# Performance work log

Hardware: AMD Instinct MI355X
Metric: run time of the kernel (lower is better)

The kernel has to match this reference:

```python
import jax, jax.numpy as jnp
import numpy as np

N = 100_000   # nodes
D = 128       # feature dim (dim_in == dim_out, residual requires it)
E = 1_600_000 # edges
T = 4         # num_layers; edge_attr (hop distance) in 1..T


def setup_inputs() -> dict:
    key = jax.random.key(0)
    k0, k1, k2, k3, k4 = jax.random.split(key, 5)
    x = jax.random.normal(k0, (N, D), dtype=jnp.float32)
    edge_index = jax.random.randint(k1, (2, E), 0, N, dtype=jnp.int32)
    edge_attr = jax.random.randint(k2, (E,), 1, T + 1, dtype=jnp.int32)  # hop k in [1, T]
    W = jax.random.normal(k3, (T, D, D), dtype=jnp.float32) * (1.0 / np.sqrt(D))
    nu = jax.random.normal(k4, (T, T), dtype=jnp.float32) * 0.1  # nu[k-1, t]
    return {"x": x, "edge_index": edge_index, "edge_attr": edge_attr, "W": W, "nu": nu}


def _gcn_edge_coef(edge_index, mask, n):
    """Symmetric GCN normalization 1/sqrt(deg_src*deg_dst) restricted to masked edges."""
    src, dst = edge_index[0], edge_index[1]
    deg_s = jax.ops.segment_sum(mask, src, num_segments=n)
    deg_d = jax.ops.segment_sum(mask, dst, num_segments=n)
    inv = lambda d: jnp.where(d > 0, jax.lax.rsqrt(jnp.maximum(d, 1.0)), 0.0)
    return mask * inv(deg_s)[src] * inv(deg_d)[dst]  # [E]


def reference(x, edge_index, edge_attr, W, nu):
    n = x.shape[0]
    T_layers = nu.shape[1]
    src, dst = edge_index[0], edge_index[1]
    # Precompute per-hop normalized edge coefficients (A(k) masks as weights -> static shapes)
    coefs = [_gcn_edge_coef(edge_index, (edge_attr == k).astype(x.dtype), n)
             for k in range(1, T_layers + 1)]
    hist = [x]  # x_t history
    for t in range(T_layers):
        acc = jnp.zeros_like(x)
        for k in range(1, t + 2):  # k = 1 .. t+1
            h = hist[t + 1 - k] @ W[k - 1]                      # [N, D] linear
            msg = h[src] * coefs[k - 1][:, None]                # gather + weight [E, D]
            agg = jax.ops.segment_sum(msg, dst, num_segments=n) # scatter-sum [N, D]
            acc = acc + nu[k - 1, t] * agg
        xt = hist[t] + jax.nn.relu(acc)                         # residual + ReLU
        # F.normalize(p=2, dim=-1), eps=1e-12 (cfg.gnn.l2norm assumed True)
        xt = xt / jnp.maximum(jnp.linalg.norm(xt, axis=-1, keepdims=True), 1e-12)
        hist.append(xt)
    return hist[-1]
```

## Files before the change

kernel.cpp:

```cpp
#include <hip/hip_runtime.h>

#define DD 128
#define NP 256
#define EB 4096

typedef float4 f4;
typedef __attribute__((ext_vector_type(8))) short bf16x8;
typedef __attribute__((ext_vector_type(4))) float f32x4;

__device__ __forceinline__ short toBf(float f) {
    unsigned u = __float_as_uint(f);
    u += 0x7fff + ((u >> 16) & 1);
    return (short)(u >> 16);
}


__global__ __launch_bounds__(1024) void kAF(const int* __restrict__ ei, int E, int PSZ, int nbA,
                                            int* __restrict__ cntB_D, int* __restrict__ cntB_S,
                                            const float* __restrict__ W, ushort* __restrict__ WT,
                                            int totW, int nPW,
                                            const float* __restrict__ x, ushort* __restrict__ xb,
                                            int n8) {
    __shared__ int hd[NP], hs[NP];
    int tid = threadIdx.x, b = blockIdx.x;
    if (b < nbA) {
        if (tid < NP) { hd[tid] = 0; hs[tid] = 0; }
        __syncthreads();
        int base = b * EB;
        int lim = min(base + EB, E);
        for (int e = base + tid; e < lim; e += 1024) {
            int s = ei[e], d = ei[E + e];
            atomicAdd(&hs[s / PSZ], 1);
            atomicAdd(&hd[d / PSZ], 1);
        }
        __syncthreads();
        if (tid < NP) {
            cntB_D[tid * nbA + b] = hd[tid];
            cntB_S[tid * nbA + b] = hs[tid];
        }
    } else if (b < nbA + nPW) {
        int i = (b - nbA) * 1024 + tid;
        if (i < totW) {
            int k = i >> 14, rem = i & 16383, j = rem >> 7, d = rem & 127;
            WT[i] = (ushort)toBf(W[(size_t)k * 16384 + (size_t)d * DD + j]);
        }
    } else {
        int i = (b - nbA - nPW) * 1024 + tid;
        if (i < n8) {
            const f4* q = (const f4*)(x + (size_t)i * 8);
            f4 lo = q[0], hi = q[1];
            bf16x8 r;
            r[0] = toBf(lo.x); r[1] = toBf(lo.y); r[2] = toBf(lo.z); r[3] = toBf(lo.w);
            r[4] = toBf(hi.x); r[5] = toBf(hi.y); r[6] = toBf(hi.z); r[7] = toBf(hi.w);
            *(bf16x8*)(xb + (size_t)i * 8) = r;
        }
    }
}

__global__ __launch_bounds__(512) void kB1(int* __restrict__ cntB_D, int* __restrict__ cntB_S,
                                           int nbA,
                                           int* __restrict__ partTotD, int* __restrict__ partTotS) {
    __shared__ int sh[512];
    int b = blockIdx.x, tid = threadIdx.x;
    int* cntB = (b < NP) ? cntB_D : cntB_S;
    int* partTot = (b < NP) ? partTotD : partTotS;
    int p = (b < NP) ? b : b - NP;
    int v = (tid < nbA) ? cntB[p * nbA + tid] : 0;
    sh[tid] = v; __syncthreads();
    for (int off = 1; off < 512; off <<= 1) {
        int add = (tid >= off) ? sh[tid - off] : 0;
        __syncthreads(); sh[tid] += add; __syncthreads();
    }
    if (tid < nbA) cntB[p * nbA + tid] = sh[tid] - v;
    if (tid == 511) partTot[p] = sh[511];
}

__global__ __launch_bounds__(1024) void kC(const int* __restrict__ ei, const int* __restrict__ ea,
                                           int E, int N, int T, int PSZ, int nbA,
                                           const int* __restrict__ cntB_D, const int* __restrict__ cntB_S,
                                           const int* __restrict__ partTotD,
                                           const int* __restrict__ partTotS,
                                           int* __restrict__ binD, ushort* __restrict__ binS) {
    __shared__ int pd[NP], ps[NP];
    __shared__ int sc[512];
    int tid = threadIdx.x, b = blockIdx.x;
    if (tid < 512) sc[tid] = (tid < 256) ? partTotD[tid] : partTotS[tid - 256];
    __syncthreads();
    for (int off = 1; off < 256; off <<= 1) {
        int add = 0;
        if (tid < 512 && (tid & 255) >= off) add = sc[tid - off];
        __syncthreads();
        if (tid < 512) sc[tid] += add;
        __syncthreads();
    }
    if (tid < NP) {
        pd[tid] = cntB_D[tid * nbA + b] + (sc[tid] - partTotD[tid]);
        ps[tid] = cntB_S[tid * nbA + b] + (sc[tid + 256] - partTotS[tid]);
    }
    __syncthreads();
    int base = b * EB;
    int lim = min(base + EB, E);
    for (int e = base + tid; e < lim; e += 1024) {
        int s = ei[e], d = ei[E + e], k = ea[e] - 1;
        int dp = d / PSZ, sp = s / PSZ;
        int loc = (d - dp * PSZ) * T + k;
        int posD = atomicAdd(&pd[dp], 1);
        binD[posD] = (loc << 21) | (k << 19) | (k * N + s);
        int posS = atomicAdd(&ps[sp], 1);
        binS[posS] = (ushort)((s - sp * PSZ) * T + k);
    }
}

__global__ __launch_bounds__(512) void kDE(const int* __restrict__ binD,
                                           const ushort* __restrict__ binS,
                                           const int* __restrict__ partTotD,
                                           const int* __restrict__ partTotS,
                                           int N, int T, int PSZ, int M, int E,
                                           int* __restrict__ rowptr, float* __restrict__ isdD2,
                                           int* __restrict__ ep, float* __restrict__ isdS) {
    __shared__ int cnt[4096];
    __shared__ int part[512];
    __shared__ int sc[256];
    int b = blockIdx.x, tid = threadIdx.x;
    bool isD = b < NP;
    int p = isD ? b : b - NP;
    const int* pt = isD ? partTotD : partTotS;
    if (tid < 256) sc[tid] = pt[tid];
    __syncthreads();
    for (int off = 1; off < 256; off <<= 1) {
        int add = (tid < 256 && tid >= off) ? sc[tid - off] : 0;
        __syncthreads();
        if (tid < 256) sc[tid] += add;
        __syncthreads();
    }
    int b1 = sc[p];
    int b0 = b1 - pt[p];
    __syncthreads();
    int nloc = PSZ * T;
    for (int i = tid; i < nloc; i += 512) cnt[i] = 0;
    __syncthreads();
    if (isD) {
        for (int e = b0 + tid; e < b1; e += 512)
            atomicAdd(&cnt[((unsigned)binD[e]) >> 21], 1);
        __syncthreads();
        int CH = (nloc + 511) / 512;
        int c0 = tid * CH, c1 = min(c0 + CH, nloc);
        int s = 0;
        for (int i = c0; i < c1; i++) s += cnt[i];
        part[tid] = s; __syncthreads();
        for (int off = 1; off < 512; off <<= 1) {
            int add = (tid >= off) ? part[tid - off] : 0;
            __syncthreads(); part[tid] += add; __syncthreads();
        }
        int run = ((tid == 0) ? 0 : part[tid - 1]) + b0;
        int gb_base = p * PSZ * T;
        for (int i = c0; i < c1; i++) {
            int v = cnt[i];
            cnt[i] = run;
            int gb = gb_base + i;
            if (gb < M) {
                rowptr[gb] = run;
                isdD2[gb] = rsqrtf((float)max(v, 1));
            }
            run += v;
        }
        __syncthreads();
        for (int e = b0 + tid; e < b1; e += 512) {
            int v = binD[e];
            int pos = atomicAdd(&cnt[((unsigned)v) >> 21], 1);
            ep[pos] = v & 0x1FFFFF;
        }
        if (p == 0 && tid == 0) rowptr[M] = E;
    } else {
        for (int e = b0 + tid; e < b1; e += 512)
            atomicAdd(&cnt[(int)binS[e]], 1);
        __syncthreads();
        int s0 = p * PSZ;
        for (int i = tid; i < nloc; i += 512) {
            int sl = i / T, k = i - sl * T;
            int snode = s0 + sl;
            if (snode < N) isdS[k * N + snode] = rsqrtf((float)max(cnt[i], 1));
        }
    }
}


__global__ __launch_bounds__(256) void k_gemm_multi(
        const ushort* __restrict__ A, const ushort* __restrict__ WTb,
        const float* __restrict__ iskb,
        ushort* __restrict__ d0, ushort* __restrict__ d1,
        ushort* __restrict__ d2, ushort* __restrict__ d3,
        int nk, int N) {
    __shared__ ushort lW[128 * 128];
    int tid = threadIdx.x;
    int wave = tid >> 6;
    int lane = tid & 63;
    int rlo = lane & 15;
    int khi = lane >> 4;
    int r0 = blockIdx.x * 128 + wave * 32;

    int ca[2];
#pragma unroll
    for (int s = 0; s < 2; s++) {
        int r = r0 + s * 16 + rlo;
        ca[s] = r < N ? r : N - 1;
    }
    bf16x8 a[2][4];
#pragma unroll
    for (int s = 0; s < 2; s++)
#pragma unroll
        for (int kk = 0; kk < 4; kk++)
            a[s][kk] = *(const bf16x8*)(A + (size_t)ca[s] * DD + kk * 32 + khi * 8);

#pragma unroll
    for (int i = 0; i < 4; i++) {
        if (i >= nk) break;
        ushort* H = (i == 0) ? d0 : (i == 1) ? d1 : (i == 2) ? d2 : d3;
        const ushort* WT = WTb + (size_t)i * DD * DD;
        const float* isk = iskb + (size_t)i * N;

        __syncthreads();
#pragma unroll
        for (int g8 = 0; g8 < 8; g8++) {
            int g = tid + g8 * 256;
            int row = g >> 4, slot = g & 15;
            bf16x8 v = *(const bf16x8*)(WT + row * DD + slot * 8);
            *(bf16x8*)(lW + row * DD + (slot ^ (row & 7)) * 8) = v;
        }
        __syncthreads();

        f32x4 acc[2][8];
#pragma unroll
        for (int s = 0; s < 2; s++)
#pragma unroll
            for (int j = 0; j < 8; j++) acc[s][j] = (f32x4){0.f, 0.f, 0.f, 0.f};

#pragma unroll
        for (int kk = 0; kk < 4; kk++) {
            int q = kk * 4 + khi;
#pragma unroll
            for (int cg = 0; cg < 8; cg++) {
                int row = cg * 16 + rlo;
                bf16x8 b = *(const bf16x8*)(lW + row * DD + (q ^ (rlo & 7)) * 8);
#pragma unroll
                for (int s = 0; s < 2; s++)
                    acc[s][cg] = __builtin_amdgcn_mfma_f32_16x16x32_bf16(a[s][kk], b, acc[s][cg], 0, 0, 0);
            }
        }

#pragma unroll
        for (int s = 0; s < 2; s++) {
#pragma unroll
            for (int r = 0; r < 4; r++) {
                int row = r0 + s * 16 + khi * 4 + r;
                if (row < N) {
                    float sc = isk[row];
#pragma unroll
                    for (int cg = 0; cg < 8; cg++)
                        H[(size_t)row * DD + cg * 16 + rlo] = (ushort)toBf(sc * acc[s][cg][r]);
                }
            }
        }
    }
}


struct APtrs { const ushort* a0; const ushort* a1; const ushort* a2; const ushort* a3; };

__global__ __launch_bounds__(256) void k_gemm_batch(APtrs ap,
                                                    const ushort* __restrict__ WTb,
                                                    const float* __restrict__ iskb,
                                                    ushort* __restrict__ Hb, int N) {
    __shared__ ushort lW[128 * 128];
    int k0 = blockIdx.y;
    const ushort* A = (k0 == 0) ? ap.a0 : (k0 == 1) ? ap.a1 : (k0 == 2) ? ap.a2 : ap.a3;
    const ushort* WT = WTb + (size_t)k0 * DD * DD;
    const float* isk = iskb + (size_t)k0 * N;
    ushort* H = Hb + (size_t)k0 * N * DD;

    int tid = threadIdx.x;
#pragma unroll
    for (int i = 0; i < 8; i++) {
        int g = tid + i * 256;
        int row = g >> 4, slot = g & 15;
        bf16x8 v = *(const bf16x8*)(WT + row * DD + slot * 8);
        *(bf16x8*)(lW + row * DD + (slot ^ (row & 7)) * 8) = v;
    }
    __syncthreads();

    int wave = tid >> 6;
    int lane = tid & 63;
    int rlo = lane & 15;
    int khi = lane >> 4;
    int r0 = blockIdx.x * 256 + wave * 64;

    f32x4 acc[4][8];
#pragma unroll
    for (int s = 0; s < 4; s++)
#pragma unroll
        for (int j = 0; j < 8; j++) acc[s][j] = (f32x4){0.f, 0.f, 0.f, 0.f};

    int ca[4];
#pragma unroll
    for (int s = 0; s < 4; s++) {
        int r = r0 + s * 16 + rlo;
        ca[s] = r < N ? r : N - 1;
    }

#pragma unroll
    for (int kk = 0; kk < 4; kk++) {
        int d0 = kk * 32 + khi * 8;
        bf16x8 a[4];
#pragma unroll
        for (int s = 0; s < 4; s++)
            a[s] = *(const bf16x8*)(A + (size_t)ca[s] * DD + d0);
        int q = kk * 4 + khi;
#pragma unroll
        for (int cg = 0; cg < 8; cg++) {
            int row = cg * 16 + rlo;
            bf16x8 b = *(const bf16x8*)(lW + row * DD + (q ^ (rlo & 7)) * 8);
#pragma unroll
            for (int s = 0; s < 4; s++)
                acc[s][cg] = __builtin_amdgcn_mfma_f32_16x16x32_bf16(a[s], b, acc[s][cg], 0, 0, 0);
        }
    }

#pragma unroll
    for (int s = 0; s < 4; s++) {
#pragma unroll
        for (int r = 0; r < 4; r++) {
            int row = r0 + s * 16 + khi * 4 + r;
            if (row < N) {
                float sc = isk[row];
#pragma unroll
                for (int cg = 0; cg < 8; cg++)
                    H[(size_t)row * DD + cg * 16 + rlo] = (ushort)toBf(sc * acc[s][cg][r]);
            }
        }
    }
}


__device__ __forceinline__ float selw(float w0, float w1, float w2, float w3, int k) {
    float a = (k & 1) ? w1 : w0;
    float b = (k & 1) ? w3 : w2;
    return (k & 2) ? b : a;
}

__global__ __launch_bounds__(256) void k_agg_fin(
        const ushort* __restrict__ H,
        const int* __restrict__ ep,
        const int* __restrict__ rp,
        const float* __restrict__ isdD2,
        const float* __restrict__ nu, int t, int T, int nk,
        const ushort* __restrict__ hp,
        ushort* __restrict__ hnB,
        float* __restrict__ outF,
        int N) {
    int node = (blockIdx.x * blockDim.x + threadIdx.x) >> 5;
    if (node >= N) return;
    int lane = threadIdx.x & 31;
    int rbase = node * T;
    int b0 = rp[rbase], b1 = rp[rbase + nk];

    float w0 = nu[t] * isdD2[rbase];
    float w1 = (1 < nk) ? nu[T + t]     * isdD2[rbase + 1] : 0.f;
    float w2 = (2 < nk) ? nu[2 * T + t] * isdD2[rbase + 2] : 0.f;
    float w3 = (3 < nk) ? nu[3 * T + t] * isdD2[rbase + 3] : 0.f;

    const char* Hc = (const char*)H;
    unsigned lb = (unsigned)lane << 3;

    float sx = 0.f, sy = 0.f, sz = 0.f, sw = 0.f;
    int e = b0;

#define DEC(P, O, C) \
    O = ((((unsigned)(P)) & 0x7FFFFu) << 8) | lb; \
    C = selw(w0, w1, w2, w3, (P) >> 19);

#define ACC(G, C) { \
    float f0 = __uint_as_float((G).x << 16); \
    float f1 = __uint_as_float((G).x & 0xffff0000u); \
    float f2 = __uint_as_float((G).y << 16); \
    float f3 = __uint_as_float((G).y & 0xffff0000u); \
    sx = fmaf((C), f0, sx); sy = fmaf((C), f1, sy); \
    sz = fmaf((C), f2, sz); sw = fmaf((C), f3, sw); }

    for (; e + 7 < b1; e += 8) {
        int p0 = ep[e],     p1 = ep[e + 1], p2 = ep[e + 2], p3 = ep[e + 3];
        int p4 = ep[e + 4], p5 = ep[e + 5], p6 = ep[e + 6], p7 = ep[e + 7];
        unsigned o0, o1, o2, o3, o4, o5, o6, o7;
        float c0, c1, c2, c3, c4, c5, c6, c7;
        DEC(p0, o0, c0) DEC(p1, o1, c1) DEC(p2, o2, c2) DEC(p3, o3, c3)
        DEC(p4, o4, c4) DEC(p5, o5, c5) DEC(p6, o6, c6) DEC(p7, o7, c7)
        uint2 g0 = *(const uint2*)(Hc + o0);
        uint2 g1 = *(const uint2*)(Hc + o1);
        uint2 g2 = *(const uint2*)(Hc + o2);
        uint2 g3 = *(const uint2*)(Hc + o3);
        uint2 g4 = *(const uint2*)(Hc + o4);
        uint2 g5 = *(const uint2*)(Hc + o5);
        uint2 g6 = *(const uint2*)(Hc + o6);
        uint2 g7 = *(const uint2*)(Hc + o7);
        ACC(g0, c0) ACC(g1, c1) ACC(g2, c2) ACC(g3, c3)
        ACC(g4, c4) ACC(g5, c5) ACC(g6, c6) ACC(g7, c7)
    }
    if (e + 3 < b1) {
        int p0 = ep[e], p1 = ep[e + 1], p2 = ep[e + 2], p3 = ep[e + 3];
        unsigned o0, o1, o2, o3;
        float c0, c1, c2, c3;
        DEC(p0, o0, c0) DEC(p1, o1, c1) DEC(p2, o2, c2) DEC(p3, o3, c3)
        uint2 g0 = *(const uint2*)(Hc + o0);
        uint2 g1 = *(const uint2*)(Hc + o1);
        uint2 g2 = *(const uint2*)(Hc + o2);
        uint2 g3 = *(const uint2*)(Hc + o3);
        ACC(g0, c0) ACC(g1, c1) ACC(g2, c2) ACC(g3, c3)
        e += 4;
    }
    for (; e < b1; e++) {
        int p0 = ep[e];
        unsigned o0; float c0;
        DEC(p0, o0, c0)
        uint2 g0 = *(const uint2*)(Hc + o0);
        ACC(g0, c0)
    }
#undef DEC
#undef ACC

    unsigned nodeOff = ((unsigned)node << 8) | lb;
    uint2 hv = *(const uint2*)((const char*)hp + nodeOff);
    float vx = __uint_as_float(hv.x << 16)         + fmaxf(sx, 0.f);
    float vy = __uint_as_float(hv.x & 0xffff0000u) + fmaxf(sy, 0.f);
    float vz = __uint_as_float(hv.y << 16)         + fmaxf(sz, 0.f);
    float vw = __uint_as_float(hv.y & 0xffff0000u) + fmaxf(sw, 0.f);
    float ss = vx * vx + vy * vy + vz * vz + vw * vw;
#pragma unroll
    for (int off = 16; off; off >>= 1) ss += __shfl_xor(ss, off, 32);
    float inv = 1.f / fmaxf(sqrtf(ss), 1e-12f);
    vx *= inv; vy *= inv; vz *= inv; vw *= inv;
    if (outF) {
        f4 o; o.x = vx; o.y = vy; o.z = vz; o.w = vw;
        *(f4*)((char*)outF + (((size_t)node << 9) | ((size_t)lane << 4))) = o;
    } else {
        uint lo = ((unsigned)(unsigned short)toBf(vx)) | (((unsigned)(unsigned short)toBf(vy)) << 16);
        uint hi = ((unsigned)(unsigned short)toBf(vz)) | (((unsigned)(unsigned short)toBf(vw)) << 16);
        uint2 ob; ob.x = lo; ob.y = hi;
        *(uint2*)((char*)hnB + nodeOff) = ob;
    }
}


extern "C" void kernel_launch(void* const* d_in, const int* in_sizes, int n_in,
                              void* d_out, int out_size, void* d_ws, size_t ws_size,
                              hipStream_t stream) {
    const float* x  = (const float*)d_in[0];
    const int*   ei = (const int*)d_in[1];
    const int*   ea = (const int*)d_in[2];
    const float* W  = (const float*)d_in[3];
    const float* nu = (const float*)d_in[4];
    float* out = (float*)d_out;

    int N = in_sizes[0] / DD;
    int E = in_sizes[1] / 2;
    int T = in_sizes[3] / (DD * DD);
    int M = T * N;
    size_t ND = (size_t)N * DD;

    int PSZ = (N + NP - 1) / NP;
    if (PSZ * T > 2048) return;
    if ((long)T * N > (1L << 19)) return;
    int nbA = (E + EB - 1) / EB;
    if (nbA > 512) return;

    size_t reqSerial = sizeof(float) * 2 * (size_t)M
                     + sizeof(ushort) * ((size_t)(4 + T) * ND + (size_t)T * DD * DD)
                     + sizeof(int) * ((size_t)M + 1 + (size_t)E + 64);
    size_t reqEager  = sizeof(float) * 2 * (size_t)M
                     + sizeof(ushort) * ((size_t)(4 + 10) * ND + (size_t)T * DD * DD)
                     + sizeof(int) * ((size_t)M + 1 + (size_t)E + 64);
    if (ws_size < reqSerial) return;
    bool eager = (T == 4) && (ws_size >= reqEager);
    size_t Lslices = eager ? 10 : (size_t)T;

    float*  isdS  = (float*)d_ws;
    float*  isdD2 = isdS + M;
    ushort* xb    = (ushort*)(isdD2 + M);
    ushort* h1b   = xb + ND;
    ushort* h2b   = h1b + ND;
    ushort* h3b   = h2b + ND;
    ushort* Lr    = h3b + ND;
    ushort* WT    = Lr + Lslices * ND;
    int* rowptr   = (int*)(WT + (size_t)T * DD * DD);
    int* ep       = rowptr + M + 1;
    int*    binD     = (int*)Lr;
    ushort* binS     = (ushort*)(binD + E);
    int*    cntB_D   = (int*)(binS + (((size_t)E + 1) & ~(size_t)1));
    int*    cntB_S   = cntB_D + NP * nbA;
    int*    partTotD = cntB_S + NP * nbA;
    int*    partTotS = partTotD + NP;

    size_t scratch = 4 * (size_t)E + 2 * ((size_t)E + 2)
                   + sizeof(int) * (2 * (size_t)NP * nbA + 2 * NP + 16);
    if (scratch > sizeof(ushort) * Lslices * ND) return;

    int totW = T * DD * DD;
    int nPW = (totW + 1023) / 1024;
    int n8 = (int)(ND / 8);
    int nCvt = (n8 + 1023) / 1024;

    kAF<<<nbA + nPW + nCvt, 1024, 0, stream>>>(ei, E, PSZ, nbA, cntB_D, cntB_S,
                                               W, WT, totW, nPW, x, xb, n8);
    kB1<<<2 * NP, 512, 0, stream>>>(cntB_D, cntB_S, nbA, partTotD, partTotS);
    kC<<<nbA, 1024, 0, stream>>>(ei, ea, E, N, T, PSZ, nbA, cntB_D, cntB_S,
                                 partTotD, partTotS, binD, binS);
    kDE<<<2 * NP, 512, 0, stream>>>(binD, binS, partTotD, partTotS,
                                    N, T, PSZ, M, E, rowptr, isdD2, ep, isdS);

    const ushort* histB[4] = {xb, h1b, h2b, h3b};
    int nodeBlocks = ((size_t)N * 32 + 255) / 256;

    if (eager) {
        ushort* L[4];
        L[0] = Lr;
        L[1] = Lr + 1 * ND;
        L[2] = Lr + 3 * ND;
        L[3] = Lr + 6 * ND;
        int gb128 = (N + 127) / 128;
        for (int t = 0; t < 4; t++) {
            int nk = 4 - t;
            ushort* d0 = L[t] + 0 * ND;
            ushort* d1 = (nk > 1) ? L[t + 1] + 1 * ND : d0;
            ushort* d2 = (nk > 2) ? L[t + 2] + 2 * ND : d0;
            ushort* d3 = (nk > 3) ? L[t + 3] + 3 * ND : d0;
            k_gemm_multi<<<gb128, 256, 0, stream>>>(histB[t], WT, isdS,
                                                    d0, d1, d2, d3, nk, N);
            bool lastL = (t == 3);
            k_agg_fin<<<nodeBlocks, 256, 0, stream>>>(L[t], ep, rowptr, isdD2,
                                                      nu, t, T, t + 1, histB[t],
                                                      lastL ? nullptr : (ushort*)histB[t + 1],
                                                      lastL ? out : nullptr, N);
        }
    } else {
        int gb256 = (N + 255) / 256;
        for (int t = 0; t < T; t++) {
            APtrs ap;
            ap.a0 = histB[t];
            ap.a1 = (t >= 1) ? histB[t - 1] : histB[0];
            ap.a2 = (t >= 2) ? histB[t - 2] : histB[0];
            ap.a3 = (t >= 3) ? histB[t - 3] : histB[0];
            dim3 grid(gb256, t + 1);
            k_gemm_batch<<<grid, 256, 0, stream>>>(ap, WT, isdS, Lr, N);
            bool lastL = (t == T - 1);
            k_agg_fin<<<nodeBlocks, 256, 0, stream>>>(Lr, ep, rowptr, isdD2,
                                                      nu, t, T, t + 1, histB[t],
                                                      lastL ? nullptr : (ushort*)histB[t + 1],
                                                      lastL ? out : nullptr, N);
        }
    }
}
```

Measured before the change: 406.9 us.

## Remap eager projection slices into six reusable buffers with per-hop base offsets

The eager path used to keep ten precomputed projection slices. It now keeps six and reuses slots through a static slot-assignment table. Edge entries now store only the source id and hop, and the aggregation kernel adds a per-hop base offset passed in as an int4, so any slot can serve any hop. This shrinks the workspace footprint and may improve L2/MALL locality for the gathers, at the cost of a select per edge. An empty marker kernel launch is also added, probably for profiling.

Result: no change. 409.3 us (+0.6%).

```diff
diff --git a/kernel.cpp b/kernel.cpp
--- a/kernel.cpp
+++ b/kernel.cpp
@@ -105,7 +105,7 @@
         int dp = d / PSZ, sp = s / PSZ;
         int loc = (d - dp * PSZ) * T + k;
         int posD = atomicAdd(&pd[dp], 1);
-        binD[posD] = (loc << 21) | (k << 19) | (k * N + s);
+        binD[posD] = (loc << 21) | (k << 17) | s;
         int posS = atomicAdd(&ps[sp], 1);
         binS[posS] = (ushort)((s - sp * PSZ) * T + k);
     }
@@ -346,9 +346,15 @@
     float b = (k & 1) ? w3 : w2;
     return (k & 2) ? b : a;
 }
+__device__ __forceinline__ int selwi(int a, int b, int c, int d, int k) {
+    int x = (k & 1) ? b : a;
+    int y = (k & 1) ? d : c;
+    return (k & 2) ? y : x;
+}
 
 __global__ __launch_bounds__(256) void k_agg_fin(
         const ushort* __restrict__ H,
+        int4 sb,
         const int* __restrict__ ep,
         const int* __restrict__ rp,
         const float* __restrict__ isdD2,
@@ -374,9 +380,10 @@
     float sx = 0.f, sy = 0.f, sz = 0.f, sw = 0.f;
     int e = b0;
 
-#define DEC(P, O, C) \
-    O = ((((unsigned)(P)) & 0x7FFFFu) << 8) | lb; \
-    C = selw(w0, w1, w2, w3, (P) >> 19);
+#define DEC(P, O, C) { \
+    int kk_ = (P) >> 17; \
+    O = (unsigned)selwi(sb.x, sb.y, sb.z, sb.w, kk_) + (((((unsigned)(P)) & 0x1FFFFu) << 8) | lb); \
+    C = selw(w0, w1, w2, w3, kk_); }
 
 #define ACC(G, C) { \
     float f0 = __uint_as_float((G).x << 16); \
@@ -448,6 +455,8 @@
     }
 }
 
+__global__ void kMark() {}
+
 
 extern "C" void kernel_launch(void* const* d_in, const int* in_sizes, int n_in,
                               void* d_out, int out_size, void* d_ws, size_t ws_size,
@@ -467,19 +476,17 @@
 
     int PSZ = (N + NP - 1) / NP;
     if (PSZ * T > 2048) return;
-    if ((long)T * N > (1L << 19)) return;
+    if (T > 4 || N > 131072) return;
     int nbA = (E + EB - 1) / EB;
     if (nbA > 512) return;
 
     size_t reqSerial = sizeof(float) * 2 * (size_t)M
-                     + sizeof(ushort) * ((size_t)(4 + T) * ND + (size_t)T * DD * DD)
+                     + sizeof(ushort) * ((size_t)(4 + 4) * ND + (size_t)T * DD * DD)
                      + sizeof(int) * ((size_t)M + 1 + (size_t)E + 64);
-    size_t reqEager  = sizeof(float) * 2 * (size_t)M
-                     + sizeof(ushort) * ((size_t)(4 + 10) * ND + (size_t)T * DD * DD)
-                     + sizeof(int) * ((size_t)M + 1 + (size_t)E + 64);
+    size_t reqEager  = reqSerial + sizeof(ushort) * 2 * ND;
     if (ws_size < reqSerial) return;
     bool eager = (T == 4) && (ws_size >= reqEager);
-    size_t Lslices = eager ? 10 : (size_t)T;
+    size_t Lslices = eager ? 6 : 4;
 
     float*  isdS  = (float*)d_ws;
     float*  isdD2 = isdS + M;
@@ -517,30 +524,36 @@
 
     const ushort* histB[4] = {xb, h1b, h2b, h3b};
     int nodeBlocks = ((size_t)N * 32 + 255) / 256;
+    int rowBytes = N * 256;
 
     if (eager) {
-        ushort* L[4];
-        L[0] = Lr;
-        L[1] = Lr + 1 * ND;
-        L[2] = Lr + 3 * ND;
-        L[3] = Lr + 6 * ND;
+        kMark<<<1, 64, 0, stream>>>();
+        const int dstSlot[4][4] = {{0, 1, 2, 3}, {4, 5, 0, 0}, {1, 4, 0, 0}, {2, 0, 0, 0}};
+        const int aggSlot[4][4] = {{0, 0, 0, 0}, {4, 1, 0, 0}, {1, 5, 2, 0}, {2, 4, 0, 3}};
         int gb128 = (N + 127) / 128;
         for (int t = 0; t < 4; t++) {
             int nk = 4 - t;
-            ushort* d0 = L[t] + 0 * ND;
-            ushort* d1 = (nk > 1) ? L[t + 1] + 1 * ND : d0;
-            ushort* d2 = (nk > 2) ? L[t + 2] + 2 * ND : d0;
-            ushort* d3 = (nk > 3) ? L[t + 3] + 3 * ND : d0;
+            ushort* d0 = Lr + (size_t)dstSlot[t][0] * ND;
+            ushort* d1 = (nk > 1) ? Lr + (size_t)dstSlot[t][1] * ND : d0;
+            ushort* d2 = (nk > 2) ? Lr + (size_t)dstSlot[t][2] * ND : d0;
+            ushort* d3 = (nk > 3) ? Lr + (size_t)dstSlot[t][3] * ND : d0;
             k_gemm_multi<<<gb128, 256, 0, stream>>>(histB[t], WT, isdS,
                                                     d0, d1, d2, d3, nk, N);
+            int4 sb;
+            sb.x = aggSlot[t][0] * rowBytes;
+            sb.y = aggSlot[t][1] * rowBytes;
+            sb.z = aggSlot[t][2] * rowBytes;
+            sb.w = aggSlot[t][3] * rowBytes;
             bool lastL = (t == 3);
-            k_agg_fin<<<nodeBlocks, 256, 0, stream>>>(L[t], ep, rowptr, isdD2,
+            k_agg_fin<<<nodeBlocks, 256, 0, stream>>>(Lr, sb, ep, rowptr, isdD2,
                                                       nu, t, T, t + 1, histB[t],
                                                       lastL ? nullptr : (ushort*)histB[t + 1],
                                                       lastL ? out : nullptr, N);
         }
     } else {
         int gb256 = (N + 255) / 256;
+        int4 sb;
+        sb.x = 0; sb.y = rowBytes; sb.z = 2 * rowBytes; sb.w = 3 * rowBytes;
         for (int t = 0; t < T; t++) {
             APtrs ap;
             ap.a0 = histB[t];
@@ -550,7 +563,7 @@
             dim3 grid(gb256, t + 1);
             k_gemm_batch<<<grid, 256, 0, stream>>>(ap, WT, isdS, Lr, N);
             bool lastL = (t == T - 1);
-            k_agg_fin<<<nodeBlocks, 256, 0, stream>>>(Lr, ep, rowptr, isdD2,
+            k_agg_fin<<<nodeBlocks, 256, 0, stream>>>(Lr, sb, ep, rowptr, isdD2,
                                                       nu, t, T, t + 1, histB[t],
                                                       lastL ? nullptr : (ushort*)histB[t + 1],
                                                       lastL ? out : nullptr, N);
```
